# Performance work log

Hardware: AMD Instinct MI355X
Metric: run time of the kernel (lower is better)

## Reference

```python
import jax, jax.numpy as jnp
import numpy as np

NEG_SLOPE = 0.2
BN_EPS = 1e-5


def setup_inputs() -> dict:
    key = jax.random.key(0)
    ks = jax.random.split(key, 12)
    N, E, F_IN, H, C, G, LAT = 50000, 1600000, 128, 2, 64, 512, 32
    x = jax.random.normal(ks[0], (N, F_IN), dtype=jnp.float32)
    edge_index = jax.random.randint(ks[1], (2, E), 0, N, dtype=jnp.int64)
    batch = jnp.sort(jax.random.randint(ks[2], (N,), 0, G, dtype=jnp.int64))
    # GATConv params (PyG layout): lin is Linear(F_IN, H*C, bias=False)
    lin_w = jax.random.normal(ks[3], (H * C, F_IN), dtype=jnp.float32) / np.sqrt(F_IN)
    att_src = jax.random.normal(ks[4], (1, H, C), dtype=jnp.float32) / np.sqrt(C)
    att_dst = jax.random.normal(ks[5], (1, H, C), dtype=jnp.float32) / np.sqrt(C)
    bias = jnp.zeros((H * C,), dtype=jnp.float32)
    bn_gamma = jnp.ones((H * C,), dtype=jnp.float32)
    bn_beta = jnp.zeros((H * C,), dtype=jnp.float32)
    fc_w = jax.random.normal(ks[6], (LAT, H * C), dtype=jnp.float32) / np.sqrt(H * C)
    fc_b = jnp.zeros((LAT,), dtype=jnp.float32)
    return {"x": x, "edge_index": edge_index, "batch": batch, "num_graphs": G,
            "lin_w": lin_w, "att_src": att_src, "att_dst": att_dst, "bias": bias,
            "bn_gamma": bn_gamma, "bn_beta": bn_beta, "fc_w": fc_w, "fc_b": fc_b}


def _gat_conv(x, src, dst, lin_w, att_src, att_dst, bias):
    N = x.shape[0]
    H, C = att_src.shape[1], att_src.shape[2]
    h = (x @ lin_w.T).reshape(N, H, C)                     # [N,H,C]
    a_src = (h * att_src).sum(-1)                          # [N,H]
    a_dst = (h * att_dst).sum(-1)                          # [N,H]
    e = a_src[src] + a_dst[dst]                            # [E,H]
    e = jnp.where(e > 0, e, NEG_SLOPE * e)                 # leaky_relu(0.2)
    # segment softmax over incoming edges of each dst node
    m = jax.ops.segment_max(e, dst, num_segments=N)        # [N,H]
    p = jnp.exp(e - m[dst])
    s = jax.ops.segment_sum(p, dst, num_segments=N)        # [N,H]
    alpha = p / s[dst]                                     # [E,H]
    msg = h[src] * alpha[:, :, None]                       # [E,H,C]
    out = jax.ops.segment_sum(msg, dst, num_segments=N)    # [N,H,C]
    return out.reshape(N, H * C) + bias


def reference(x, edge_index, batch, num_graphs, lin_w, att_src, att_dst, bias,
              bn_gamma, bn_beta, fc_w, fc_b):
    N = x.shape[0]
    loops = jnp.arange(N, dtype=edge_index.dtype)
    src = jnp.concatenate([edge_index[0], loops])          # add_self_loops=True
    dst = jnp.concatenate([edge_index[1], loops])
    h = _gat_conv(x, src, dst, lin_w, att_src, att_dst, bias)
    pooled = jax.ops.segment_sum(h, batch, num_segments=num_graphs)  # [G, H*C]
    mu = pooled.mean(0)
    var = pooled.var(0)
    out = (pooled - mu) / jnp.sqrt(var + BN_EPS) * bn_gamma + bn_beta
    return out @ fc_w.T + fc_b
```

## Files before the change

### kernel.cpp

```cpp
#include <hip/hip_runtime.h>
#include <hip/hip_bf16.h>


#define BKT_SHIFT 8
#define BKT_MASK  255
#define BKT_CAP   14336
#define BIN_TILE  4096

typedef __attribute__((ext_vector_type(8))) short bf16x8;
typedef __attribute__((ext_vector_type(4))) float f32x4;

static __device__ __forceinline__ float lo16(unsigned int u) {
    union { unsigned int i; float f; } c; c.i = u << 16; return c.f;
}
static __device__ __forceinline__ float hi16(unsigned int u) {
    union { unsigned int i; float f; } c; c.i = u & 0xffff0000u; return c.f;
}
static __device__ __forceinline__ unsigned short f2bf(float f) {
    unsigned int b = __builtin_bit_cast(unsigned int, f);
    return (unsigned short)((b >> 16) + ((b >> 15) & 1));
}
static __device__ __forceinline__ float rlane_f(float x, int l) {
    return __builtin_bit_cast(float, __builtin_amdgcn_readlane(__builtin_bit_cast(int, x), l));
}

__global__ void k_prep(float* __restrict__ zp, long long nz,
                       const float* __restrict__ w, unsigned short* __restrict__ wb) {
    long long i = (long long)blockIdx.x * blockDim.x + threadIdx.x;
    long long stride = (long long)gridDim.x * blockDim.x;
    for (long long k = i; k < nz; k += stride) zp[k] = 0.f;
    for (long long k = i; k < 128 * 128; k += stride) wb[k] = f2bf(w[k]);
}

__global__ __launch_bounds__(256) void k_linhist(const float* __restrict__ x,
                                                 const unsigned short* __restrict__ wb,
                                                 const float* __restrict__ att_s,
                                                 const float* __restrict__ att_d,
                                                 unsigned short* __restrict__ h2,
                                                 float* __restrict__ asrc,
                                                 float* __restrict__ adst, int N,
                                                 const int* __restrict__ ei, int E,
                                                 int* __restrict__ blkhist,
                                                 int NB, int nlin) {
    const int t = threadIdx.x;
    if ((int)blockIdx.x >= nlin) {
        __shared__ int cnt[1024];
        int hb = blockIdx.x - nlin;
        for (int i = t; i < 1024; i += 256) cnt[i] = 0;
        __syncthreads();
        int base = hb * BIN_TILE;
        int end = min(base + BIN_TILE, E);
        for (int i = base + t; i < end; i += 256)
            atomicAdd(&cnt[ei[E + i] >> BKT_SHIFT], 1);
        __syncthreads();
        int* row = blkhist + (size_t)hb * NB;
        for (int b = t; b < NB; b += 256) row[b] = cnt[b];
        return;
    }
    const int lane = t & 63;
    const int wid = t >> 6;
    const int row0 = (blockIdx.x * 4 + wid) * 16;
    const int rlo = lane & 15;
    const int khi = lane >> 4;

    int arow = row0 + rlo; if (arow >= N) arow = N - 1;
    const float* xrow = x + (long long)arow * 128;
    bf16x8 afrag[4];
#pragma unroll
    for (int ks = 0; ks < 4; ++ks) {
        int k0 = ks * 32 + khi * 8;
        float4 xa = *(const float4*)(xrow + k0);
        float4 xb = *(const float4*)(xrow + k0 + 4);
        bf16x8 a;
        a[0] = (short)f2bf(xa.x); a[1] = (short)f2bf(xa.y);
        a[2] = (short)f2bf(xa.z); a[3] = (short)f2bf(xa.w);
        a[4] = (short)f2bf(xb.x); a[5] = (short)f2bf(xb.y);
        a[6] = (short)f2bf(xb.z); a[7] = (short)f2bf(xb.w);
        afrag[ks] = a;
    }

    float ps0[4] = {0.f,0.f,0.f,0.f}, pd0[4] = {0.f,0.f,0.f,0.f};
    float ps1[4] = {0.f,0.f,0.f,0.f}, pd1[4] = {0.f,0.f,0.f,0.f};

    for (int ct = 0; ct < 8; ++ct) {
        const int col = ct * 16 + rlo;
        f32x4 acc = {0.f, 0.f, 0.f, 0.f};
#pragma unroll
        for (int ks = 0; ks < 4; ++ks) {
            bf16x8 b = *(const bf16x8*)(wb + (size_t)col * 128 + ks * 32 + khi * 8);
            acc = __builtin_amdgcn_mfma_f32_16x16x32_bf16(afrag[ks], b, acc, 0, 0, 0);
        }
        const float as = att_s[col], ad = att_d[col];
        const bool head0 = (ct < 4);
#pragma unroll
        for (int r = 0; r < 4; ++r) {
            int row = row0 + khi * 4 + r;
            if (row < N) h2[(long long)row * 128 + col] = f2bf(acc[r]);
            float v = acc[r];
            if (head0) { ps0[r] = fmaf(v, as, ps0[r]); pd0[r] = fmaf(v, ad, pd0[r]); }
            else       { ps1[r] = fmaf(v, as, ps1[r]); pd1[r] = fmaf(v, ad, pd1[r]); }
        }
    }

#pragma unroll
    for (int off = 1; off <= 8; off <<= 1) {
#pragma unroll
        for (int r = 0; r < 4; ++r) {
            ps0[r] += __shfl_xor(ps0[r], off);
            pd0[r] += __shfl_xor(pd0[r], off);
            ps1[r] += __shfl_xor(ps1[r], off);
            pd1[r] += __shfl_xor(pd1[r], off);
        }
    }
    if (rlo == 0) {
#pragma unroll
        for (int r = 0; r < 4; ++r) {
            int row = row0 + khi * 4 + r;
            if (row < N) {
                asrc[row * 2]     = ps0[r];
                asrc[row * 2 + 1] = ps1[r];
                adst[row * 2]     = pd0[r];
                adst[row * 2 + 1] = pd1[r];
            }
        }
    }
}

__global__ __launch_bounds__(256) void k_scanA(int* __restrict__ blkhist,
                                               int* __restrict__ tot,
                                               int NB, int nbin) {
    int b = blockIdx.x * 4 + (threadIdx.x >> 6);
    int lane = threadIdx.x & 63;
    if (b >= NB) return;
    int run = 0;
    for (int blk0 = 0; blk0 < nbin; blk0 += 64) {
        int idx = blk0 + lane;
        int v = (idx < nbin) ? blkhist[(size_t)idx * NB + b] : 0;
        int inc = v;
#pragma unroll
        for (int off = 1; off < 64; off <<= 1) {
            int u = __shfl_up(inc, off);
            if (lane >= off) inc += u;
        }
        if (idx < nbin) blkhist[(size_t)idx * NB + b] = run + (inc - v);
        run += __shfl(inc, 63);
    }
    if (lane == 0) tot[b] = run;
}

__global__ __launch_bounds__(256) void k_bin(const int* __restrict__ ei, int E,
                                             const int* __restrict__ blkhist,
                                             const int* __restrict__ tot,
                                             unsigned int* __restrict__ stage, int NB) {
    __shared__ int gb[1024];
    __shared__ int cnt[1024];
    __shared__ int part[256];
    int t = threadIdx.x;
    const int* row = blkhist + (size_t)blockIdx.x * NB;
    int vals[4]; int s0 = 0;
#pragma unroll
    for (int k = 0; k < 4; ++k) {
        int b2 = t * 4 + k;
        vals[k] = (b2 < NB) ? tot[b2] : 0;
        s0 += vals[k];
    }
    part[t] = s0;
    __syncthreads();
    for (int off = 1; off < 256; off <<= 1) {
        int u = (t >= off) ? part[t - off] : 0;
        __syncthreads();
        part[t] += u;
        __syncthreads();
    }
    int base = part[t] - s0;
#pragma unroll
    for (int k = 0; k < 4; ++k) {
        int b2 = t * 4 + k;
        if (b2 < NB) { gb[b2] = base + row[b2]; cnt[b2] = 0; }
        base += vals[k];
    }
    __syncthreads();
    int ebase = blockIdx.x * BIN_TILE;
    int eend = min(ebase + BIN_TILE, E);
    for (int i = ebase + t; i < eend; i += 256) {
        int s = ei[i];
        int d = ei[E + i];
        int b = d >> BKT_SHIFT;
        int off = atomicAdd(&cnt[b], 1);
        stage[gb[b] + off] = ((unsigned int)(d & BKT_MASK) << 24) | (unsigned int)s;
    }
}

__global__ __launch_bounds__(256) void k_bsort(const int* __restrict__ tot,
                                               const unsigned int* __restrict__ stage,
                                               int* __restrict__ rowptr,
                                               int* __restrict__ csr,
                                               int N, int E, int NB) {
    __shared__ int hist[256];
    __shared__ int sc[256];
    __shared__ int rp[256];
    __shared__ int lc[256];
    __shared__ int part[256];
    __shared__ int s_bb, s_be;
    __shared__ int lout[BKT_CAP];
    int b = blockIdx.x;
    int node0 = b << BKT_SHIFT;
    int nloc = min(256, N - node0);
    int t = threadIdx.x;

    int vals[4]; int s0 = 0;
#pragma unroll
    for (int k = 0; k < 4; ++k) {
        int b2 = t * 4 + k;
        vals[k] = (b2 < NB) ? tot[b2] : 0;
        s0 += vals[k];
    }
    part[t] = s0;
    __syncthreads();
    for (int off = 1; off < 256; off <<= 1) {
        int u = (t >= off) ? part[t - off] : 0;
        __syncthreads();
        part[t] += u;
        __syncthreads();
    }
    int base = part[t] - s0;
#pragma unroll
    for (int k = 0; k < 4; ++k) {
        int b2 = t * 4 + k;
        if (b2 == b) { s_bb = base; s_be = base + vals[k]; }
        base += vals[k];
    }
    __syncthreads();
    const int bb = s_bb, be = s_be;

    hist[t] = 0; lc[t] = 0;
    __syncthreads();
    for (int i = bb + t; i < be; i += 256)
        atomicAdd(&hist[stage[i] >> 24], 1);
    __syncthreads();
    sc[t] = hist[t];
    __syncthreads();
    for (int off = 1; off < 256; off <<= 1) {
        int u = (t >= off) ? sc[t - off] : 0;
        __syncthreads();
        sc[t] += u;
        __syncthreads();
    }
    int rpg = bb + sc[t] - hist[t];
    rp[t] = rpg;
    if (t < nloc) rowptr[node0 + t] = rpg;
    if (b == 0 && t == 0) rowptr[N] = E;
    __syncthreads();
    for (int i = bb + t; i < be; i += 256) {
        unsigned int wrec = stage[i];
        int dl = (int)(wrec >> 24);
        int src = (int)(wrec & 0x00FFFFFFu);
        int pos = rp[dl] + atomicAdd(&lc[dl], 1);
        int rel = pos - bb;
        if (rel < BKT_CAP) lout[rel] = src;
        else csr[pos] = src;
    }
    __syncthreads();
    int cntb = be - bb; if (cntb > BKT_CAP) cntb = BKT_CAP;
    for (int i = t; i < cntb; i += 256) csr[bb + i] = lout[i];
}

__global__ __launch_bounds__(256) void k_agg(const int* __restrict__ rowptr,
                                             const int* __restrict__ csr_src,
                                             const unsigned short* __restrict__ h2,
                                             const float* __restrict__ asrc,
                                             const float* __restrict__ adst,
                                             const float* __restrict__ bias,
                                             const int* __restrict__ batch,
                                             float* __restrict__ pooled, int N) {
    int n = __builtin_amdgcn_readfirstlane(blockIdx.x * 4 + (threadIdx.x >> 6));
    const int lane = threadIdx.x & 63;
    if (n >= N) return;
    const bool lo = (lane < 32);
    const int el = lane & 31;

    float2 adn = *(const float2*)(adst + (size_t)n * 2);
    float2 asn = *(const float2*)(asrc + (size_t)n * 2);
    float e0 = asn.x + adn.x; e0 = e0 > 0.f ? e0 : 0.2f * e0;
    float e1 = asn.y + adn.y; e1 = e1 > 0.f ? e1 : 0.2f * e1;
    float w0 = __expf(e0), w1 = __expf(e1);

    unsigned int v = ((const unsigned int*)(h2 + (size_t)n * 128))[lane];
    float wh = lo ? w0 : w1;
    float aX = wh * lo16(v), aY = wh * hi16(v);
    float ps = 0.f;
    const float adh = lo ? adn.x : adn.y;

    const int beg = rowptr[n], end = rowptr[n + 1];
    for (int base = beg; base < end; base += 32) {
        int cnt = min(32, end - base);
        int sv = n;
        if (el < cnt) sv = csr_src[base + el];
        float av = asrc[(size_t)sv * 2 + (lo ? 0 : 1)];
        float f = av + adh; f = f > 0.f ? f : 0.2f * f;
        float usel = (el < cnt) ? __expf(f) : 0.f;
        ps += usel;

        int k = 0;
        for (; k + 8 <= cnt; k += 8) {
#pragma unroll
            for (int j = 0; j < 8; ++j) {
                int e = k + j;
                int se = __builtin_amdgcn_readlane(sv, e);
                float su0 = rlane_f(usel, e);
                float su1 = rlane_f(usel, e + 32);
                float uu = lo ? su0 : su1;
                unsigned int vv = ((const unsigned int*)(h2 + (size_t)se * 128))[lane];
                aX = fmaf(uu, lo16(vv), aX);
                aY = fmaf(uu, hi16(vv), aY);
            }
        }
        for (; k < cnt; ++k) {
            int se = __builtin_amdgcn_readlane(sv, k);
            float su0 = rlane_f(usel, k);
            float su1 = rlane_f(usel, k + 32);
            float uu = lo ? su0 : su1;
            unsigned int vv = ((const unsigned int*)(h2 + (size_t)se * 128))[lane];
            aX = fmaf(uu, lo16(vv), aX);
            aY = fmaf(uu, hi16(vv), aY);
        }
    }

#pragma unroll
    for (int off = 1; off <= 16; off <<= 1)
        ps += __shfl_xor(ps, off);
    float sdiv = ps + (lo ? w0 : w1);

    int j0 = lane * 2;
    float2 bv = *(const float2*)(bias + j0);
    float o0 = aX / sdiv + bv.x;
    float o1 = aY / sdiv + bv.y;
    int g = batch[n];
    atomicAdd(&pooled[(size_t)g * 128 + j0], o0);
    atomicAdd(&pooled[(size_t)g * 128 + j0 + 1], o1);
}

__global__ __launch_bounds__(512) void k_bnstat(const float* __restrict__ pooled,
                                                const float* __restrict__ gamma,
                                                const float* __restrict__ beta,
                                                float* __restrict__ scale,
                                                float* __restrict__ shift, int G) {
    __shared__ float ls[512], lq[512];
    int t = threadIdx.x;
    int j = t & 127, q = t >> 7;
    int per = G >> 2;
    float sum = 0.f, sq = 0.f;
    for (int g = q * per; g < (q + 1) * per; ++g) {
        float v = pooled[g * 128 + j];
        sum += v; sq += v * v;
    }
    ls[t] = sum; lq[t] = sq;
    __syncthreads();
    if (t < 128) {
        sum = ls[t] + ls[t + 128] + ls[t + 256] + ls[t + 384];
        sq  = lq[t] + lq[t + 128] + lq[t + 256] + lq[t + 384];
        float mu = sum / (float)G;
        float var = sq / (float)G - mu * mu;
        float sc = gamma[t] * rsqrtf(var + 1e-5f);
        scale[t] = sc;
        shift[t] = beta[t] - mu * sc;
    }
}

__global__ __launch_bounds__(128) void k_fc(const float* __restrict__ pooled,
                                            const float* __restrict__ scale,
                                            const float* __restrict__ shift,
                                            const float* __restrict__ fcw,
                                            const float* __restrict__ fcb,
                                            float* __restrict__ out, int LAT) {
    __shared__ float nrm[128];
    int g = blockIdx.x;
    int t = threadIdx.x;
    nrm[t] = pooled[g * 128 + t] * scale[t] + shift[t];
    __syncthreads();
    if (t < LAT) {
        float acc = fcb[t];
#pragma unroll 8
        for (int j = 0; j < 128; ++j)
            acc = fmaf(nrm[j], fcw[t * 128 + j], acc);
        out[g * LAT + t] = acc;
    }
}

extern "C" void kernel_launch(void* const* d_in, const int* in_sizes, int n_in,
                              void* d_out, int out_size, void* d_ws, size_t ws_size,
                              hipStream_t stream) {
    const float* x     = (const float*)d_in[0];
    const int*   ei    = (const int*)d_in[1];
    const int*   batch = (const int*)d_in[2];
    const float* lin_w = (const float*)d_in[4];
    const float* att_s = (const float*)d_in[5];
    const float* att_d = (const float*)d_in[6];
    const float* bias  = (const float*)d_in[7];
    const float* gamma = (const float*)d_in[8];
    const float* beta  = (const float*)d_in[9];
    const float* fcw   = (const float*)d_in[10];
    const float* fcb   = (const float*)d_in[11];
    float* out = (float*)d_out;

    const int N   = in_sizes[2];
    const int E   = in_sizes[1] / 2;
    const int LAT = in_sizes[11];
    const int G   = out_size / LAT;
    const int NB  = (N + 255) >> BKT_SHIFT;
    const int nbin = (E + BIN_TILE - 1) / BIN_TILE;
    const int nlin = (N + 63) / 64;

    char* ws = (char*)d_ws;
    unsigned short* h2 = (unsigned short*)ws; ws += (size_t)N * 128 * 2;
    unsigned short* wb = (unsigned short*)ws; ws += (size_t)128 * 128 * 2;
    float* asrc   = (float*)ws; ws += (size_t)N * 2 * 4;
    float* adst   = (float*)ws; ws += (size_t)N * 2 * 4;
    float* pooled = (float*)ws; ws += (size_t)G * 128 * 4;
    float* scale  = (float*)ws; ws += 128 * 4;
    float* shift  = (float*)ws; ws += 128 * 4;
    int*   tot    = (int*)ws;   ws += (size_t)NB * 4;
    int*   blkhist= (int*)ws;   ws += (size_t)nbin * NB * 4;
    int*   rowptr = (int*)ws;   ws += (size_t)(N + 1) * 4;
    unsigned int* stage = (unsigned int*)ws; ws += (size_t)E * 4;
    int*   csr    = (int*)ws;   ws += (size_t)E * 4;

    k_prep<<<128, 256, 0, stream>>>(pooled, (long long)G * 128, lin_w, wb);
    k_linhist<<<nlin + nbin, 256, 0, stream>>>(x, wb, att_s, att_d, h2, asrc, adst, N,
                                               ei, E, blkhist, NB, nlin);
    k_scanA<<<(NB + 3) / 4, 256, 0, stream>>>(blkhist, tot, NB, nbin);
    k_bin<<<nbin, 256, 0, stream>>>(ei, E, blkhist, tot, stage, NB);
    k_bsort<<<NB, 256, 0, stream>>>(tot, stage, rowptr, csr, N, E, NB);
    k_agg<<<(N + 3) / 4, 256, 0, stream>>>(rowptr, csr, h2, asrc, adst, bias, batch, pooled, N);
    k_bnstat<<<1, 512, 0, stream>>>(pooled, gamma, beta, scale, shift, G);
    k_fc<<<G, 128, 0, stream>>>(pooled, scale, shift, fcw, fcb, out, LAT);
}
```

Before: 182.7 us.

## Regroup kernel stages to cut launches: fuse hist+prep, lin+scan, bn+fc

The launch sequence is reorganised from 8 kernels into 6. The edge histogram moves into the prep kernel, the column scan runs alongside the linear transform, and batch-norm statistics and the final FC are merged into a single one-block kernel. The aim is to cut launch overhead and the serial gaps between small kernels. The risk is that the FC step, 512x32 dot products of length 128, now runs on one 512-thread block instead of 512 blocks, which may serialise that work.

```diff
diff --git a/kernel.cpp b/kernel.cpp
--- a/kernel.cpp
+++ b/kernel.cpp
@@ -24,37 +24,63 @@
     return __builtin_bit_cast(float, __builtin_amdgcn_readlane(__builtin_bit_cast(int, x), l));
 }
 
-__global__ void k_prep(float* __restrict__ zp, long long nz,
-                       const float* __restrict__ w, unsigned short* __restrict__ wb) {
-    long long i = (long long)blockIdx.x * blockDim.x + threadIdx.x;
-    long long stride = (long long)gridDim.x * blockDim.x;
-    for (long long k = i; k < nz; k += stride) zp[k] = 0.f;
-    for (long long k = i; k < 128 * 128; k += stride) wb[k] = f2bf(w[k]);
-}
-
-__global__ __launch_bounds__(256) void k_linhist(const float* __restrict__ x,
+__global__ __launch_bounds__(256) void k_histprep(const int* __restrict__ ei, int E,
+                                                  int* __restrict__ blkhist, int NB,
+                                                  const float* __restrict__ w,
+                                                  unsigned short* __restrict__ wb,
+                                                  float* __restrict__ pooled,
+                                                  long long npool, int nbin) {
+    const int t = threadIdx.x;
+    const int bid = blockIdx.x;
+    if (bid < nbin) {
+        __shared__ int cnt[1024];
+        for (int i = t; i < 1024; i += 256) cnt[i] = 0;
+        __syncthreads();
+        int base = bid * BIN_TILE;
+        int end = min(base + BIN_TILE, E);
+        for (int i = base + t; i < end; i += 256)
+            atomicAdd(&cnt[ei[E + i] >> BKT_SHIFT], 1);
+        __syncthreads();
+        int* row = blkhist + (size_t)bid * NB;
+        for (int b = t; b < NB; b += 256) row[b] = cnt[b];
+    } else if (bid < nbin + 64) {
+        int i = (bid - nbin) * 256 + t;
+        wb[i] = f2bf(w[i]);
+    } else {
+        long long i = (long long)(bid - nbin - 64) * 256 + t;
+        for (; i < npool; i += 64 * 256) pooled[i] = 0.f;
+    }
+}
+
+__global__ __launch_bounds__(256) void k_linscan(const float* __restrict__ x,
                                                  const unsigned short* __restrict__ wb,
                                                  const float* __restrict__ att_s,
                                                  const float* __restrict__ att_d,
                                                  unsigned short* __restrict__ h2,
                                                  float* __restrict__ asrc,
                                                  float* __restrict__ adst, int N,
-                                                 const int* __restrict__ ei, int E,
                                                  int* __restrict__ blkhist,
-                                                 int NB, int nlin) {
+                                                 int* __restrict__ tot,
+                                                 int NB, int nbin, int nlin) {
     const int t = threadIdx.x;
     if ((int)blockIdx.x >= nlin) {
-        __shared__ int cnt[1024];
-        int hb = blockIdx.x - nlin;
-        for (int i = t; i < 1024; i += 256) cnt[i] = 0;
-        __syncthreads();
-        int base = hb * BIN_TILE;
-        int end = min(base + BIN_TILE, E);
-        for (int i = base + t; i < end; i += 256)
-            atomicAdd(&cnt[ei[E + i] >> BKT_SHIFT], 1);
-        __syncthreads();
-        int* row = blkhist + (size_t)hb * NB;
-        for (int b = t; b < NB; b += 256) row[b] = cnt[b];
+        int b = (blockIdx.x - nlin) * 4 + (t >> 6);
+        int lane = t & 63;
+        if (b >= NB) return;
+        int run = 0;
+        for (int blk0 = 0; blk0 < nbin; blk0 += 64) {
+            int idx = blk0 + lane;
+            int v = (idx < nbin) ? blkhist[(size_t)idx * NB + b] : 0;
+            int inc = v;
+#pragma unroll
+            for (int off = 1; off < 64; off <<= 1) {
+                int u = __shfl_up(inc, off);
+                if (lane >= off) inc += u;
+            }
+            if (idx < nbin) blkhist[(size_t)idx * NB + b] = run + (inc - v);
+            run += __shfl(inc, 63);
+        }
+        if (lane == 0) tot[b] = run;
         return;
     }
     const int lane = t & 63;
@@ -124,28 +150,6 @@
             }
         }
     }
-}
-
-__global__ __launch_bounds__(256) void k_scanA(int* __restrict__ blkhist,
-                                               int* __restrict__ tot,
-                                               int NB, int nbin) {
-    int b = blockIdx.x * 4 + (threadIdx.x >> 6);
-    int lane = threadIdx.x & 63;
-    if (b >= NB) return;
-    int run = 0;
-    for (int blk0 = 0; blk0 < nbin; blk0 += 64) {
-        int idx = blk0 + lane;
-        int v = (idx < nbin) ? blkhist[(size_t)idx * NB + b] : 0;
-        int inc = v;
-#pragma unroll
-        for (int off = 1; off < 64; off <<= 1) {
-            int u = __shfl_up(inc, off);
-            if (lane >= off) inc += u;
-        }
-        if (idx < nbin) blkhist[(size_t)idx * NB + b] = run + (inc - v);
-        run += __shfl(inc, 63);
-    }
-    if (lane == 0) tot[b] = run;
 }
 
 __global__ __launch_bounds__(256) void k_bin(const int* __restrict__ ei, int E,
@@ -340,12 +344,14 @@
     atomicAdd(&pooled[(size_t)g * 128 + j0 + 1], o1);
 }
 
-__global__ __launch_bounds__(512) void k_bnstat(const float* __restrict__ pooled,
-                                                const float* __restrict__ gamma,
-                                                const float* __restrict__ beta,
-                                                float* __restrict__ scale,
-                                                float* __restrict__ shift, int G) {
+__global__ __launch_bounds__(512) void k_bnfc(const float* __restrict__ pooled,
+                                              const float* __restrict__ gamma,
+                                              const float* __restrict__ beta,
+                                              const float* __restrict__ fcw,
+                                              const float* __restrict__ fcb,
+                                              float* __restrict__ out, int G, int LAT) {
     __shared__ float ls[512], lq[512];
+    __shared__ float sscale[128], sshift[128];
     int t = threadIdx.x;
     int j = t & 127, q = t >> 7;
     int per = G >> 2;
@@ -362,28 +368,21 @@
         float mu = sum / (float)G;
         float var = sq / (float)G - mu * mu;
         float sc = gamma[t] * rsqrtf(var + 1e-5f);
-        scale[t] = sc;
-        shift[t] = beta[t] - mu * sc;
-    }
-}
-
-__global__ __launch_bounds__(128) void k_fc(const float* __restrict__ pooled,
-                                            const float* __restrict__ scale,
-                                            const float* __restrict__ shift,
-                                            const float* __restrict__ fcw,
-                                            const float* __restrict__ fcb,
-                                            float* __restrict__ out, int LAT) {
-    __shared__ float nrm[128];
-    int g = blockIdx.x;
-    int t = threadIdx.x;
-    nrm[t] = pooled[g * 128 + t] * scale[t] + shift[t];
-    __syncthreads();
-    if (t < LAT) {
-        float acc = fcb[t];
+        sscale[t] = sc;
+        sshift[t] = beta[t] - mu * sc;
+    }
+    __syncthreads();
+    int total = G * LAT;
+    for (int o = t; o < total; o += 512) {
+        int g = o / LAT;
+        int l = o - g * LAT;
+        const float* pg = pooled + (size_t)g * 128;
+        const float* wl = fcw + (size_t)l * 128;
+        float acc = fcb[l];
 #pragma unroll 8
-        for (int j = 0; j < 128; ++j)
-            acc = fmaf(nrm[j], fcw[t * 128 + j], acc);
-        out[g * LAT + t] = acc;
+        for (int j2 = 0; j2 < 128; ++j2)
+            acc = fmaf(pg[j2] * sscale[j2] + sshift[j2], wl[j2], acc);
+        out[o] = acc;
     }
 }
 
@@ -417,21 +416,19 @@
     float* asrc   = (float*)ws; ws += (size_t)N * 2 * 4;
     float* adst   = (float*)ws; ws += (size_t)N * 2 * 4;
     float* pooled = (float*)ws; ws += (size_t)G * 128 * 4;
-    float* scale  = (float*)ws; ws += 128 * 4;
-    float* shift  = (float*)ws; ws += 128 * 4;
     int*   tot    = (int*)ws;   ws += (size_t)NB * 4;
     int*   blkhist= (int*)ws;   ws += (size_t)nbin * NB * 4;
     int*   rowptr = (int*)ws;   ws += (size_t)(N + 1) * 4;
     unsigned int* stage = (unsigned int*)ws; ws += (size_t)E * 4;
     int*   csr    = (int*)ws;   ws += (size_t)E * 4;
 
-    k_prep<<<128, 256, 0, stream>>>(pooled, (long long)G * 128, lin_w, wb);
-    k_linhist<<<nlin + nbin, 256, 0, stream>>>(x, wb, att_s, att_d, h2, asrc, adst, N,
-                                               ei, E, blkhist, NB, nlin);
-    k_scanA<<<(NB + 3) / 4, 256, 0, stream>>>(blkhist, tot, NB, nbin);
+    k_histprep<<<nbin + 128, 256, 0, stream>>>(ei, E, blkhist, NB, lin_w, wb,
+                                               pooled, (long long)G * 128, nbin);
+    k_linscan<<<nlin + (NB + 3) / 4, 256, 0, stream>>>(x, wb, att_s, att_d, h2,
+                                                       asrc, adst, N, blkhist, tot,
+                                                       NB, nbin, nlin);
     k_bin<<<nbin, 256, 0, stream>>>(ei, E, blkhist, tot, stage, NB);
     k_bsort<<<NB, 256, 0, stream>>>(tot, stage, rowptr, csr, N, E, NB);
     k_agg<<<(N + 3) / 4, 256, 0, stream>>>(rowptr, csr, h2, asrc, adst, bias, batch, pooled, N);
-    k_bnstat<<<1, 512, 0, stream>>>(pooled, gamma, beta, scale, shift, G);
-    k_fc<<<G, 128, 0, stream>>>(pooled, scale, shift, fcw, fcb, out, LAT);
-}
+    k_bnfc<<<1, 512, 0, stream>>>(pooled, gamma, beta, fcw, fcb, out, G, LAT);
+}
```

After: 447.4 us. 2.45x slower.
